# Kernel optimization log

Measured on AMD Instinct MI355X. Metric: run time of the kernel, lower is better.

## Reference

```python
import jax, jax.numpy as jnp
import numpy as np

N_NODES = 100000
N_EDGES = 3200000
IN_DIM, HID_DIM, OUT_DIM = 384, 128, 5


def gcn_conv(x, src, dst, W, b, num_nodes):
    # PyG GCNConv: add self-loops, symmetric normalization, linear, aggregate, bias
    h = x @ W  # [N, out]
    ones = jnp.ones(src.shape[0], dtype=h.dtype)
    deg = jax.ops.segment_sum(ones, dst, num_segments=num_nodes)  # includes self-loops
    dinv = jnp.where(deg > 0, jax.lax.rsqrt(deg), 0.0)
    norm = dinv[src] * dinv[dst]  # [E+N]
    msg = h[src] * norm[:, None]
    out = jax.ops.segment_sum(msg, dst, num_segments=num_nodes)
    return out + b


def setup_inputs() -> dict:
    key = jax.random.key(0)
    ks = jax.random.split(key, 8)
    x = jax.random.normal(ks[0], (N_NODES, IN_DIM), dtype=jnp.float32)
    edge_index = jax.random.randint(ks[1], (2, N_EDGES), 0, N_NODES, dtype=jnp.int64)
    # Glorot-ish init for GCN linear weights
    def glorot(k, fi, fo):
        s = jnp.sqrt(6.0 / (fi + fo))
        return jax.random.uniform(k, (fi, fo), jnp.float32, -s, s)
    W1 = glorot(ks[2], IN_DIM, HID_DIM)
    b1 = jnp.zeros((HID_DIM,), jnp.float32)
    W2 = glorot(ks[3], HID_DIM, HID_DIM)
    b2 = jnp.zeros((HID_DIM,), jnp.float32)
    W3 = glorot(ks[4], HID_DIM, OUT_DIM)
    b3 = jnp.zeros((OUT_DIM,), jnp.float32)
    return {"x": x, "edge_index": edge_index, "W1": W1, "b1": b1,
            "W2": W2, "b2": b2, "W3": W3, "b3": b3}


def reference(x, edge_index, W1, b1, W2, b2, W3, b3):
    num_nodes = x.shape[0]
    loops = jnp.arange(num_nodes, dtype=edge_index.dtype)
    src = jnp.concatenate([edge_index[0], loops])
    dst = jnp.concatenate([edge_index[1], loops])
    # layer 1: GCNConv + ReLU (dropout is identity at inference)
    h = jax.nn.relu(gcn_conv(x, src, dst, W1, b1, num_nodes))
    # layer 2
    h = jax.nn.relu(gcn_conv(h, src, dst, W2, b2, num_nodes))
    # final layer: logits, no activation
    return gcn_conv(h, src, dst, W3, b3, num_nodes)
```

## Files before the change

kernel.cpp:

```cpp
#include <hip/hip_runtime.h>

#define NN 100000
#define NE 3200000
#define SCAN_CHUNK 1024

#define BSH 8
#define BKT_NODES 256
#define NBKT ((NN + BKT_NODES - 1) / BKT_NODES)
#define BIN_BLOCKS 256
#define EPB ((NE + BIN_BLOCKS - 1) / BIN_BLOCKS)
#define GH (NBKT * BIN_BLOCKS)

typedef unsigned int uint;
typedef unsigned short ushort;
typedef __attribute__((ext_vector_type(8))) short short8;
typedef __attribute__((ext_vector_type(4))) float f32x4;

__device__ inline ushort bf16rne(float x) {
    uint u = __float_as_uint(x);
    u += 0x7FFFu + ((u >> 16) & 1u);
    return (ushort)(u >> 16);
}
__device__ inline void split2(float x, ushort& h, ushort& l) {
    h = bf16rne(x);
    float hf = __uint_as_float((uint)h << 16);
    l = bf16rne(x - hf);
}
__device__ inline uint bf16pair(float a, float b) {
    uint ua = __float_as_uint(a);
    uint ub = __float_as_uint(b);
    ua += 0x7FFFu + ((ua >> 16) & 1u);
    ub += 0x7FFFu + ((ub >> 16) & 1u);
    return (ua >> 16) | (ub & 0xFFFF0000u);
}
__device__ inline float bflo(uint u) { return __uint_as_float(u << 16); }
__device__ inline float bfhi(uint u) { return __uint_as_float(u & 0xFFFF0000u); }

__global__ __launch_bounds__(256) void hist_bkt(const int* __restrict__ dst,
                                                int* __restrict__ ghist) {
    __shared__ int h[NBKT];
    int t = threadIdx.x;
    for (int i = t; i < NBKT; i += 256) h[i] = 0;
    __syncthreads();
    int beg = blockIdx.x * EPB;
    int end = beg + EPB; if (end > NE) end = NE;
    for (int e = beg + t; e < end; e += 256)
        atomicAdd(&h[dst[e] >> BSH], 1);
    __syncthreads();
    for (int i = t; i < NBKT; i += 256)
        ghist[i * BIN_BLOCKS + blockIdx.x] = h[i];
}

__global__ __launch_bounds__(256) void scan_p1(const int* __restrict__ cnt,
                                               int* __restrict__ bsum, int N) {
    int t = threadIdx.x;
    int base = blockIdx.x * SCAN_CHUNK + t * 4;
    int s = 0;
#pragma unroll
    for (int q = 0; q < 4; q++) {
        int i = base + q;
        if (i < N) s += cnt[i];
    }
    __shared__ int red[4];
#pragma unroll
    for (int off = 32; off; off >>= 1) s += __shfl_down(s, off, 64);
    if ((t & 63) == 0) red[t >> 6] = s;
    __syncthreads();
    if (t == 0) bsum[blockIdx.x] = red[0] + red[1] + red[2] + red[3];
}

__global__ void scan_p2(int* __restrict__ bsum, int nb) {
    __shared__ int s[128];
    int t = threadIdx.x;
    int v = (t < nb) ? bsum[t] : 0;
    s[t] = v;
    __syncthreads();
    for (int off = 1; off < 128; off <<= 1) {
        int x = s[t];
        int add = (t >= off) ? s[t - off] : 0;
        __syncthreads();
        s[t] = x + add;
        __syncthreads();
    }
    if (t < nb) bsum[t] = s[t] - v;
}

__global__ __launch_bounds__(256) void scan_p3_plain(int* __restrict__ data,
                                                     const int* __restrict__ bsum, int N) {
    __shared__ int ts[256];
    int t = threadIdx.x;
    int base = blockIdx.x * SCAN_CHUNK + t * 4;
    int c[4];
    int s = 0;
#pragma unroll
    for (int q = 0; q < 4; q++) {
        int i = base + q;
        c[q] = (i < N) ? data[i] : 0;
        s += c[q];
    }
    ts[t] = s;
    __syncthreads();
    for (int off = 1; off < 256; off <<= 1) {
        int x = ts[t];
        int add = (t >= off) ? ts[t - off] : 0;
        __syncthreads();
        ts[t] = x + add;
        __syncthreads();
    }
    int run = bsum[blockIdx.x] + ts[t] - s;
#pragma unroll
    for (int q = 0; q < 4; q++) {
        int i = base + q;
        if (i < N) { data[i] = run; run += c[q]; }
    }
}

__global__ __launch_bounds__(256) void scan_p3_deg(const int* __restrict__ cnt,
                                                   const int* __restrict__ bsum,
                                                   int* __restrict__ rowptr,
                                                   float* __restrict__ dinv, int N) {
    __shared__ int ts[256];
    int t = threadIdx.x;
    int base = blockIdx.x * SCAN_CHUNK + t * 4;
    int c[4];
    int s = 0;
#pragma unroll
    for (int q = 0; q < 4; q++) {
        int i = base + q;
        c[q] = (i < N) ? cnt[i] : 0;
        s += c[q];
    }
    ts[t] = s;
    __syncthreads();
    for (int off = 1; off < 256; off <<= 1) {
        int x = ts[t];
        int add = (t >= off) ? ts[t - off] : 0;
        __syncthreads();
        ts[t] = x + add;
        __syncthreads();
    }
    int run = bsum[blockIdx.x] + ts[t] - s;
#pragma unroll
    for (int q = 0; q < 4; q++) {
        int i = base + q;
        if (i < N) {
            rowptr[i] = run;
            dinv[i] = 1.0f / sqrtf((float)(c[q] + 1));
            run += c[q];
        }
    }
    if (base < N && N <= base + 4) rowptr[N] = run;
}

__global__ __launch_bounds__(256) void bin_edges(const int* __restrict__ src,
                                                 const int* __restrict__ dst,
                                                 const int* __restrict__ ghist,
                                                 uint* __restrict__ binned) {
    __shared__ int cur[NBKT];
    int t = threadIdx.x;
    for (int i = t; i < NBKT; i += 256) cur[i] = ghist[i * BIN_BLOCKS + blockIdx.x];
    __syncthreads();
    int beg = blockIdx.x * EPB;
    int end = beg + EPB; if (end > NE) end = NE;
    for (int e = beg + t; e < end; e += 256) {
        int d = dst[e];
        int b = d >> BSH;
        int p = atomicAdd(&cur[b], 1);
        binned[p] = ((uint)src[e] << BSH) | (uint)(d & (BKT_NODES - 1));
    }
}

__global__ __launch_bounds__(256) void bucket_count(const uint* __restrict__ binned,
                                                    const int* __restrict__ ghist,
                                                    int* __restrict__ cnt) {
    __shared__ int c[BKT_NODES];
    int t = threadIdx.x;
    int bkt = blockIdx.x;
    for (int i = t; i < BKT_NODES; i += 256) c[i] = 0;
    __syncthreads();
    int beg = ghist[bkt * BIN_BLOCKS];
    int end = (bkt == NBKT - 1) ? NE : ghist[(bkt + 1) * BIN_BLOCKS];
    for (int j = beg + t; j < end; j += 256)
        atomicAdd(&c[binned[j] & (BKT_NODES - 1)], 1);
    __syncthreads();
    int base = bkt * BKT_NODES;
    int nb = NN - base; if (nb > BKT_NODES) nb = BKT_NODES;
    for (int i = t; i < nb; i += 256) cnt[base + i] = c[i];
}

__global__ __launch_bounds__(256) void csr_fill(const uint* __restrict__ binned,
                                                const int* __restrict__ ghist,
                                                const int* __restrict__ rowptr,
                                                int* __restrict__ col) {
    __shared__ int fill[BKT_NODES];
    int t = threadIdx.x;
    int bkt = blockIdx.x;
    for (int i = t; i < BKT_NODES; i += 256) fill[i] = 0;
    __syncthreads();
    int beg = ghist[bkt * BIN_BLOCKS];
    int end = (bkt == NBKT - 1) ? NE : ghist[(bkt + 1) * BIN_BLOCKS];
    int base = bkt * BKT_NODES;
    for (int j = beg + t; j < end; j += 256) {
        uint r = binned[j];
        int dl = r & (BKT_NODES - 1);
        int p = rowptr[base + dl] + atomicAdd(&fill[dl], 1);
        col[p] = (int)(r >> BSH);
    }
}

template <int K>
__global__ __launch_bounds__(256) void wsplit(const float* __restrict__ W,
                                              ushort* __restrict__ Wth,
                                              ushort* __restrict__ Wtl) {
    __shared__ float tile[32][128];
    int t = threadIdx.x;
    int kb = blockIdx.x;
    {
        int k = t >> 3, cq = t & 7;
#pragma unroll
        for (int q = 0; q < 4; q++) {
            float4 v = *(const float4*)&W[(size_t)(kb * 32 + k) * 128 + cq * 16 + q * 4];
            *(float4*)&tile[k][cq * 16 + q * 4] = v;
        }
    }
    __syncthreads();
    {
        int c = t >> 1, g = t & 1;
        ushort hs[16], ls[16];
#pragma unroll
        for (int i = 0; i < 16; i++) split2(tile[g * 16 + i][c], hs[i], ls[i]);
        uint h[8], lo[8];
#pragma unroll
        for (int i = 0; i < 8; i++) {
            h[i] = (uint)hs[2 * i] | ((uint)hs[2 * i + 1] << 16);
            lo[i] = (uint)ls[2 * i] | ((uint)ls[2 * i + 1] << 16);
        }
        size_t o = (size_t)c * K + kb * 32 + g * 16;
        *(uint4*)&Wth[o] = make_uint4(h[0], h[1], h[2], h[3]);
        *(uint4*)&Wth[o + 8] = make_uint4(h[4], h[5], h[6], h[7]);
        *(uint4*)&Wtl[o] = make_uint4(lo[0], lo[1], lo[2], lo[3]);
        *(uint4*)&Wtl[o + 8] = make_uint4(lo[4], lo[5], lo[6], lo[7]);
    }
}

template <int K>
__global__ __launch_bounds__(256) void mfma_gemm(const float* __restrict__ X,
                                                 const ushort* __restrict__ Wth,
                                                 const ushort* __restrict__ Wtl,
                                                 const float* __restrict__ dinv,
                                                 uint* __restrict__ Y, int M) {
    __shared__ char smem[24 * 1024];
    char* aHi = smem;
    char* aLo = smem + 4096;
    char* bHi = smem + 8192;
    char* bLo = smem + 16384;
    int tid = threadIdx.x;
    int w = tid >> 6, l = tid & 63;
    int rowBase = blockIdx.x * 64;

    f32x4 acc[8];
#pragma unroll
    for (int n = 0; n < 8; n++) acc[n] = (f32x4){0.f, 0.f, 0.f, 0.f};

    int sRow = tid >> 2, sKg = tid & 3;
    int gRowA = rowBase + sRow;
    int fKg = l >> 4;
    int aOff = fKg * 1024 + ((16 * w + (l & 15)) ^ fKg) * 16;

    for (int kt = 0; kt < K; kt += 32) {
        {
            float v[8];
            if (gRowA < M) {
                float4 p0 = *(const float4*)&X[(size_t)gRowA * K + kt + sKg * 8];
                float4 p1 = *(const float4*)&X[(size_t)gRowA * K + kt + sKg * 8 + 4];
                v[0] = p0.x; v[1] = p0.y; v[2] = p0.z; v[3] = p0.w;
                v[4] = p1.x; v[5] = p1.y; v[6] = p1.z; v[7] = p1.w;
            } else {
#pragma unroll
                for (int i = 0; i < 8; i++) v[i] = 0.f;
            }
            uint hh[4], hl[4];
#pragma unroll
            for (int i = 0; i < 4; i++) {
                ushort h0, l0, h1, l1;
                split2(v[2 * i], h0, l0);
                split2(v[2 * i + 1], h1, l1);
                hh[i] = (uint)h0 | ((uint)h1 << 16);
                hl[i] = (uint)l0 | ((uint)l1 << 16);
            }
            int wa = sKg * 1024 + ((sRow ^ sKg) * 16);
            *(uint4*)(aHi + wa) = make_uint4(hh[0], hh[1], hh[2], hh[3]);
            *(uint4*)(aLo + wa) = make_uint4(hl[0], hl[1], hl[2], hl[3]);
        }
#pragma unroll
        for (int i = 0; i < 2; i++) {
            int ci = tid + i * 256;
            int colb = ci >> 2, kg = ci & 3;
            uint4 vh = *(const uint4*)&Wth[(size_t)colb * K + kt + kg * 8];
            uint4 vl = *(const uint4*)&Wtl[(size_t)colb * K + kt + kg * 8];
            int wb = kg * 2048 + ((colb ^ kg) * 16);
            *(uint4*)(bHi + wb) = vh;
            *(uint4*)(bLo + wb) = vl;
        }
        __syncthreads();
        short8 ah = *(const short8*)(aHi + aOff);
        short8 al = *(const short8*)(aLo + aOff);
#pragma unroll
        for (int n = 0; n < 8; n++) {
            int bOff = fKg * 2048 + ((16 * n + (l & 15)) ^ fKg) * 16;
            short8 bh = *(const short8*)(bHi + bOff);
            short8 bl = *(const short8*)(bLo + bOff);
            acc[n] = __builtin_amdgcn_mfma_f32_16x16x32_bf16(ah, bh, acc[n], 0, 0, 0);
            acc[n] = __builtin_amdgcn_mfma_f32_16x16x32_bf16(ah, bl, acc[n], 0, 0, 0);
            acc[n] = __builtin_amdgcn_mfma_f32_16x16x32_bf16(al, bh, acc[n], 0, 0, 0);
        }
        __syncthreads();
    }
    float dscale[4];
#pragma unroll
    for (int r = 0; r < 4; r++) {
        int row = rowBase + 16 * w + (l >> 4) * 4 + r;
        dscale[r] = (row < M) ? dinv[row] : 0.f;
    }
#pragma unroll
    for (int n = 0; n < 8; n++) {
#pragma unroll
        for (int r = 0; r < 4; r++) {
            float val = acc[n][r] * dscale[r];
            float p = __shfl_xor(val, 1, 64);
            int row = rowBase + 16 * w + (l >> 4) * 4 + r;
            if (!(l & 1) && row < M)
                Y[(size_t)row * 64 + 8 * n + ((l & 15) >> 1)] = bf16pair(val, p);
        }
    }
}

__global__ void gemm_n5(const float* __restrict__ X, const float* __restrict__ W,
                        float* __restrict__ Y, int M) {
    int idx = blockIdx.x * 256 + threadIdx.x;
    int row = idx / 5, c = idx % 5;
    if (row >= M) return;
    float acc = 0.f;
#pragma unroll 8
    for (int k = 0; k < 128; k++) acc += X[row * 128 + k] * W[k * 5 + c];
    Y[row * 5 + c] = acc;
}

__global__ void pack5(const float* __restrict__ Y, const float* __restrict__ dinv,
                      uint4* __restrict__ hc, int N) {
    int node = blockIdx.x * 256 + threadIdx.x;
    if (node >= N) return;
    float di = dinv[node];
    float v0 = Y[node * 5 + 0] * di;
    float v1 = Y[node * 5 + 1] * di;
    float v2 = Y[node * 5 + 2] * di;
    float v3 = Y[node * 5 + 3] * di;
    float v4 = Y[node * 5 + 4] * di;
    hc[node] = make_uint4(bf16pair(v0, v1), bf16pair(v2, v3), bf16pair(v4, 0.f), 0u);
}

#define ACC8(v)                         \
    a0 += bflo(v.x); a1 += bfhi(v.x);   \
    a2 += bflo(v.y); a3 += bfhi(v.y);   \
    a4 += bflo(v.z); a5 += bfhi(v.z);   \
    a6 += bflo(v.w); a7 += bfhi(v.w);

__global__ __launch_bounds__(256) void agg128_v3(const uint4* __restrict__ hb4,
                                                 const int* __restrict__ rowptr,
                                                 const int* __restrict__ col,
                                                 const float* __restrict__ dinv,
                                                 const float* __restrict__ bias,
                                                 float* __restrict__ out, int N, int do_relu) {
    int wave = threadIdx.x >> 6;
    int lane = threadIdx.x & 63;
    int node = blockIdx.x * 4 + wave;
    if (node >= N) return;
    int g = lane >> 4;
    int q = lane & 15;
    int beg = rowptr[node], end = rowptr[node + 1];
    float a0 = 0.f, a1 = 0.f, a2 = 0.f, a3 = 0.f, a4 = 0.f, a5 = 0.f, a6 = 0.f, a7 = 0.f;

    int j = beg;
    for (; j + 16 <= end; j += 16) {
        int s0 = col[j + g];
        int s1 = col[j + 4 + g];
        int s2 = col[j + 8 + g];
        int s3 = col[j + 12 + g];
        uint4 v0 = hb4[(size_t)s0 * 16 + q];
        uint4 v1 = hb4[(size_t)s1 * 16 + q];
        uint4 v2 = hb4[(size_t)s2 * 16 + q];
        uint4 v3 = hb4[(size_t)s3 * 16 + q];
        ACC8(v0); ACC8(v1); ACC8(v2); ACC8(v3);
    }
    if (j + 8 <= end) {
        int s0 = col[j + g];
        int s1 = col[j + 4 + g];
        uint4 v0 = hb4[(size_t)s0 * 16 + q];
        uint4 v1 = hb4[(size_t)s1 * 16 + q];
        ACC8(v0); ACC8(v1);
        j += 8;
    }
    if (j < end) {
        int jj0 = j + g, jj1 = j + 4 + g;
        bool p0 = jj0 < end, p1 = jj1 < end;
        int s0 = p0 ? col[jj0] : node;
        int s1 = p1 ? col[jj1] : node;
        uint4 v0 = hb4[(size_t)s0 * 16 + q];
        uint4 v1 = hb4[(size_t)s1 * 16 + q];
        if (!p0) v0 = make_uint4(0u, 0u, 0u, 0u);
        if (!p1) v1 = make_uint4(0u, 0u, 0u, 0u);
        ACC8(v0); ACC8(v1);
    }
#pragma unroll
    for (int off = 16; off <= 32; off <<= 1) {
        a0 += __shfl_xor(a0, off, 64);
        a1 += __shfl_xor(a1, off, 64);
        a2 += __shfl_xor(a2, off, 64);
        a3 += __shfl_xor(a3, off, 64);
        a4 += __shfl_xor(a4, off, 64);
        a5 += __shfl_xor(a5, off, 64);
        a6 += __shfl_xor(a6, off, 64);
        a7 += __shfl_xor(a7, off, 64);
    }
    if (g == 0) {
        uint4 vs = hb4[(size_t)node * 16 + q];
        ACC8(vs);
        float di = dinv[node];
        const float4* bias4 = (const float4*)bias;
        float4 bb0 = bias4[q * 2], bb1 = bias4[q * 2 + 1];
        float o0 = a0 * di + bb0.x, o1 = a1 * di + bb0.y;
        float o2 = a2 * di + bb0.z, o3 = a3 * di + bb0.w;
        float o4 = a4 * di + bb1.x, o5 = a5 * di + bb1.y;
        float o6 = a6 * di + bb1.z, o7 = a7 * di + bb1.w;
        if (do_relu) {
            o0 = fmaxf(o0, 0.f); o1 = fmaxf(o1, 0.f);
            o2 = fmaxf(o2, 0.f); o3 = fmaxf(o3, 0.f);
            o4 = fmaxf(o4, 0.f); o5 = fmaxf(o5, 0.f);
            o6 = fmaxf(o6, 0.f); o7 = fmaxf(o7, 0.f);
        }
        float4* out4 = (float4*)out;
        out4[(size_t)node * 32 + q * 2] = make_float4(o0, o1, o2, o3);
        out4[(size_t)node * 32 + q * 2 + 1] = make_float4(o4, o5, o6, o7);
    }
}

__global__ void agg5_v2(const uint4* __restrict__ hc, const int* __restrict__ rowptr,
                        const int* __restrict__ col, const float* __restrict__ dinv,
                        const float* __restrict__ b3, float* __restrict__ out, int N) {
    int node = blockIdx.x * 256 + threadIdx.x;
    if (node >= N) return;
    float a0 = 0.f, a1 = 0.f, a2 = 0.f, a3 = 0.f, a4 = 0.f;
    int beg = rowptr[node], end = rowptr[node + 1];
#pragma unroll 2
    for (int j = beg; j < end; ++j) {
        uint4 v = hc[col[j]];
        a0 += bflo(v.x); a1 += bfhi(v.x);
        a2 += bflo(v.y); a3 += bfhi(v.y);
        a4 += bflo(v.z);
    }
    uint4 vs = hc[node];
    a0 += bflo(vs.x); a1 += bfhi(vs.x);
    a2 += bflo(vs.y); a3 += bfhi(vs.y);
    a4 += bflo(vs.z);
    float di = dinv[node];
    out[node * 5 + 0] = a0 * di + b3[0];
    out[node * 5 + 1] = a1 * di + b3[1];
    out[node * 5 + 2] = a2 * di + b3[2];
    out[node * 5 + 3] = a3 * di + b3[3];
    out[node * 5 + 4] = a4 * di + b3[4];
}

static inline size_t align512(size_t x) { return (x + 511) & ~(size_t)511; }

extern "C" void kernel_launch(void* const* d_in, const int* in_sizes, int n_in,
                              void* d_out, int out_size, void* d_ws, size_t ws_size,
                              hipStream_t stream) {
    const float* x  = (const float*)d_in[0];
    const int* ei   = (const int*)d_in[1];
    const float* W1 = (const float*)d_in[2];
    const float* b1 = (const float*)d_in[3];
    const float* W2 = (const float*)d_in[4];
    const float* b2 = (const float*)d_in[5];
    const float* W3 = (const float*)d_in[6];
    const float* b3 = (const float*)d_in[7];
    const int* src = ei;
    const int* dst = ei + NE;

    char* ws = (char*)d_ws;
    size_t off = 0;
    int* cnt = (int*)(ws + off);        off += align512((size_t)NN * 4);
    int* rowptr = (int*)(ws + off);     off += align512((size_t)(NN + 1) * 4);
    float* dinv = (float*)(ws + off);   off += align512((size_t)NN * 4);
    int* bsum = (int*)(ws + off);       off += align512((size_t)128 * 4);
    int* ghist = (int*)(ws + off);      off += align512((size_t)GH * 4);
    ushort* wt1h = (ushort*)(ws + off); off += align512((size_t)128 * 384 * 2);
    ushort* wt1l = (ushort*)(ws + off); off += align512((size_t)128 * 384 * 2);
    ushort* wt2h = (ushort*)(ws + off); off += align512((size_t)128 * 128 * 2);
    ushort* wt2l = (ushort*)(ws + off); off += align512((size_t)128 * 128 * 2);
    int* col = (int*)(ws + off);        off += align512((size_t)NE * 4);
    uint* hb = (uint*)(ws + off);       off += align512((size_t)NN * 64 * 4);
    float* bufF = (float*)(ws + off);   off += align512((size_t)NN * 128 * 4);
    float* bufC = (float*)(ws + off);   off += align512((size_t)NN * 5 * 4);
    uint4* hc = (uint4*)(ws + off);     off += align512((size_t)NN * 16);
    uint* binned = (uint*)bufF;
    (void)ws_size;

    wsplit<384><<<12, 256, 0, stream>>>(W1, wt1h, wt1l);
    wsplit<128><<<4, 256, 0, stream>>>(W2, wt2h, wt2l);

    hist_bkt<<<BIN_BLOCKS, 256, 0, stream>>>(dst, ghist);
    {
        int nb = (GH + SCAN_CHUNK - 1) / SCAN_CHUNK;
        scan_p1<<<nb, 256, 0, stream>>>(ghist, bsum, GH);
        scan_p2<<<1, 128, 0, stream>>>(bsum, nb);
        scan_p3_plain<<<nb, 256, 0, stream>>>(ghist, bsum, GH);
    }
    bin_edges<<<BIN_BLOCKS, 256, 0, stream>>>(src, dst, ghist, binned);
    bucket_count<<<NBKT, 256, 0, stream>>>(binned, ghist, cnt);
    {
        int nb = (NN + SCAN_CHUNK - 1) / SCAN_CHUNK;
        scan_p1<<<nb, 256, 0, stream>>>(cnt, bsum, NN);
        scan_p2<<<1, 128, 0, stream>>>(bsum, nb);
        scan_p3_deg<<<nb, 256, 0, stream>>>(cnt, bsum, rowptr, dinv, NN);
    }
    csr_fill<<<NBKT, 256, 0, stream>>>(binned, ghist, rowptr, col);

    int gemm_blocks = (NN + 63) / 64;
    mfma_gemm<384><<<gemm_blocks, 256, 0, stream>>>(x, wt1h, wt1l, dinv, hb, NN);
    agg128_v3<<<(NN + 3) / 4, 256, 0, stream>>>((const uint4*)hb, rowptr, col, dinv, b1, bufF, NN, 1);
    mfma_gemm<128><<<gemm_blocks, 256, 0, stream>>>(bufF, wt2h, wt2l, dinv, hb, NN);
    agg128_v3<<<(NN + 3) / 4, 256, 0, stream>>>((const uint4*)hb, rowptr, col, dinv, b2, bufF, NN, 1);
    gemm_n5<<<((NN * 5) + 255) / 256, 256, 0, stream>>>(bufF, W3, bufC, NN);
    pack5<<<(NN + 255) / 256, 256, 0, stream>>>(bufC, dinv, hc, NN);
    agg5_v2<<<(NN + 255) / 256, 256, 0, stream>>>(hc, rowptr, col, dinv, b3, (float*)d_out, NN);
}
```

Measured before the change: 492.3 us.

## Enlarge GEMM row tile, prefetch A into registers, load B via global_load_lds

The split-bf16 MFMA GEMM now processes 128 rows per block, so each wave computes two 16-row fragments and every B fragment read from LDS is reused twice. The next A k-slice is prefetched into registers while MFMAs run. B tiles are copied straight from global memory into LDS with global_load_lds instead of passing through registers. The XOR swizzle is dropped in favour of an unswizzled layout, which may add LDS bank conflicts, and the larger LDS footprint and accumulator count could lower occupancy.

Measured after the change: 495.9 us. No clear change (+0.7%).

```diff
diff --git a/kernel.cpp b/kernel.cpp
--- a/kernel.cpp
+++ b/kernel.cpp
@@ -15,6 +15,12 @@
 typedef unsigned short ushort;
 typedef __attribute__((ext_vector_type(8))) short short8;
 typedef __attribute__((ext_vector_type(4))) float f32x4;
+
+__device__ inline void gload16(const void* g, void* l) {
+    __builtin_amdgcn_global_load_lds(
+        (const __attribute__((address_space(1))) void*)g,
+        (__attribute__((address_space(3))) void*)l, 16, 0, 0);
+}
 
 __device__ inline ushort bf16rne(float x) {
     uint u = __float_as_uint(x);
@@ -249,88 +255,111 @@
                                                  const ushort* __restrict__ Wtl,
                                                  const float* __restrict__ dinv,
                                                  uint* __restrict__ Y, int M) {
-    __shared__ char smem[24 * 1024];
+    __shared__ char smem[32 * 1024];
     char* aHi = smem;
-    char* aLo = smem + 4096;
-    char* bHi = smem + 8192;
-    char* bLo = smem + 16384;
+    char* aLo = smem + 8192;
+    char* bHi = smem + 16384;
+    char* bLo = smem + 24576;
     int tid = threadIdx.x;
     int w = tid >> 6, l = tid & 63;
-    int rowBase = blockIdx.x * 64;
-
-    f32x4 acc[8];
-#pragma unroll
-    for (int n = 0; n < 8; n++) acc[n] = (f32x4){0.f, 0.f, 0.f, 0.f};
-
-    int sRow = tid >> 2, sKg = tid & 3;
-    int gRowA = rowBase + sRow;
-    int fKg = l >> 4;
-    int aOff = fKg * 1024 + ((16 * w + (l & 15)) ^ fKg) * 16;
+    int rowBase = blockIdx.x * 128;
+
+    f32x4 acc[2][8];
+#pragma unroll
+    for (int mf = 0; mf < 2; mf++)
+#pragma unroll
+        for (int n = 0; n < 8; n++) acc[mf][n] = (f32x4){0.f, 0.f, 0.f, 0.f};
+
+    int sRow = tid >> 1, sKp = tid & 1;
+    int gRow = rowBase + sRow;
+    bool rowOK = gRow < M;
+    size_t aBase = (size_t)(rowOK ? gRow : 0) * K + sKp * 16;
+
+    float4 a0, a1, a2, a3;
+    a0 = a1 = a2 = a3 = make_float4(0.f, 0.f, 0.f, 0.f);
+    if (rowOK) {
+        a0 = *(const float4*)&X[aBase];
+        a1 = *(const float4*)&X[aBase + 4];
+        a2 = *(const float4*)&X[aBase + 8];
+        a3 = *(const float4*)&X[aBase + 12];
+    }
+
+    int fc = l & 15, fkg = l >> 4;
 
     for (int kt = 0; kt < K; kt += 32) {
+#pragma unroll
+        for (int i = 0; i < 2; i++) {
+            int cb = (i * 4 + w) * 64;
+            int c = cb + l;
+            int colb = c >> 2, kg = c & 3;
+            size_t go = (size_t)colb * K + kt + kg * 8;
+            gload16(&Wth[go], bHi + cb * 16);
+            gload16(&Wtl[go], bLo + cb * 16);
+        }
         {
-            float v[8];
-            if (gRowA < M) {
-                float4 p0 = *(const float4*)&X[(size_t)gRowA * K + kt + sKg * 8];
-                float4 p1 = *(const float4*)&X[(size_t)gRowA * K + kt + sKg * 8 + 4];
-                v[0] = p0.x; v[1] = p0.y; v[2] = p0.z; v[3] = p0.w;
-                v[4] = p1.x; v[5] = p1.y; v[6] = p1.z; v[7] = p1.w;
-            } else {
-#pragma unroll
-                for (int i = 0; i < 8; i++) v[i] = 0.f;
-            }
-            uint hh[4], hl[4];
-#pragma unroll
-            for (int i = 0; i < 4; i++) {
+            float v[16] = {a0.x, a0.y, a0.z, a0.w, a1.x, a1.y, a1.z, a1.w,
+                           a2.x, a2.y, a2.z, a2.w, a3.x, a3.y, a3.z, a3.w};
+            uint hh[8], hl[8];
+#pragma unroll
+            for (int i = 0; i < 8; i++) {
                 ushort h0, l0, h1, l1;
                 split2(v[2 * i], h0, l0);
                 split2(v[2 * i + 1], h1, l1);
                 hh[i] = (uint)h0 | ((uint)h1 << 16);
                 hl[i] = (uint)l0 | ((uint)l1 << 16);
             }
-            int wa = sKg * 1024 + ((sRow ^ sKg) * 16);
+            int wa = (sRow * 4 + sKp * 2) * 16;
             *(uint4*)(aHi + wa) = make_uint4(hh[0], hh[1], hh[2], hh[3]);
+            *(uint4*)(aHi + wa + 16) = make_uint4(hh[4], hh[5], hh[6], hh[7]);
             *(uint4*)(aLo + wa) = make_uint4(hl[0], hl[1], hl[2], hl[3]);
-        }
-#pragma unroll
-        for (int i = 0; i < 2; i++) {
-            int ci = tid + i * 256;
-            int colb = ci >> 2, kg = ci & 3;
-            uint4 vh = *(const uint4*)&Wth[(size_t)colb * K + kt + kg * 8];
-            uint4 vl = *(const uint4*)&Wtl[(size_t)colb * K + kt + kg * 8];
-            int wb = kg * 2048 + ((colb ^ kg) * 16);
-            *(uint4*)(bHi + wb) = vh;
-            *(uint4*)(bLo + wb) = vl;
-        }
-        __syncthreads();
-        short8 ah = *(const short8*)(aHi + aOff);
-        short8 al = *(const short8*)(aLo + aOff);
+            *(uint4*)(aLo + wa + 16) = make_uint4(hl[4], hl[5], hl[6], hl[7]);
+        }
+        __syncthreads();
+
+        if (kt + 32 < K && rowOK) {
+            size_t nb = aBase + kt + 32;
+            a0 = *(const float4*)&X[nb];
+            a1 = *(const float4*)&X[nb + 4];
+            a2 = *(const float4*)&X[nb + 8];
+            a3 = *(const float4*)&X[nb + 12];
+        }
+
+#pragma unroll
+        for (int mf = 0; mf < 2; mf++) {
+            int aoff = (((2 * w + mf) * 16 + fc) * 4 + fkg) * 16;
+            short8 ah = *(const short8*)(aHi + aoff);
+            short8 al = *(const short8*)(aLo + aoff);
+#pragma unroll
+            for (int n = 0; n < 8; n++) {
+                int boff = ((16 * n + fc) * 4 + fkg) * 16;
+                short8 bh = *(const short8*)(bHi + boff);
+                short8 bl = *(const short8*)(bLo + boff);
+                acc[mf][n] = __builtin_amdgcn_mfma_f32_16x16x32_bf16(ah, bh, acc[mf][n], 0, 0, 0);
+                acc[mf][n] = __builtin_amdgcn_mfma_f32_16x16x32_bf16(ah, bl, acc[mf][n], 0, 0, 0);
+                acc[mf][n] = __builtin_amdgcn_mfma_f32_16x16x32_bf16(al, bh, acc[mf][n], 0, 0, 0);
+            }
+        }
+        __syncthreads();
+    }
+
+#pragma unroll
+    for (int mf = 0; mf < 2; mf++) {
+        float dscale[4];
+#pragma unroll
+        for (int r = 0; r < 4; r++) {
+            int row = rowBase + (2 * w + mf) * 16 + fkg * 4 + r;
+            dscale[r] = (row < M) ? dinv[row] : 0.f;
+        }
 #pragma unroll
         for (int n = 0; n < 8; n++) {
-            int bOff = fKg * 2048 + ((16 * n + (l & 15)) ^ fKg) * 16;
-            short8 bh = *(const short8*)(bHi + bOff);
-            short8 bl = *(const short8*)(bLo + bOff);
-            acc[n] = __builtin_amdgcn_mfma_f32_16x16x32_bf16(ah, bh, acc[n], 0, 0, 0);
-            acc[n] = __builtin_amdgcn_mfma_f32_16x16x32_bf16(ah, bl, acc[n], 0, 0, 0);
-            acc[n] = __builtin_amdgcn_mfma_f32_16x16x32_bf16(al, bh, acc[n], 0, 0, 0);
-        }
-        __syncthreads();
-    }
-    float dscale[4];
-#pragma unroll
-    for (int r = 0; r < 4; r++) {
-        int row = rowBase + 16 * w + (l >> 4) * 4 + r;
-        dscale[r] = (row < M) ? dinv[row] : 0.f;
-    }
-#pragma unroll
-    for (int n = 0; n < 8; n++) {
-#pragma unroll
-        for (int r = 0; r < 4; r++) {
-            float val = acc[n][r] * dscale[r];
-            float p = __shfl_xor(val, 1, 64);
-            int row = rowBase + 16 * w + (l >> 4) * 4 + r;
-            if (!(l & 1) && row < M)
-                Y[(size_t)row * 64 + 8 * n + ((l & 15) >> 1)] = bf16pair(val, p);
+#pragma unroll
+            for (int r = 0; r < 4; r++) {
+                float val = acc[mf][n][r] * dscale[r];
+                float p = __shfl_xor(val, 1, 64);
+                int row = rowBase + (2 * w + mf) * 16 + fkg * 4 + r;
+                if (!(l & 1) && row < M)
+                    Y[(size_t)row * 64 + 8 * n + (fc >> 1)] = bf16pair(val, p);
+            }
         }
     }
 }
@@ -525,7 +554,7 @@
     }
     csr_fill<<<NBKT, 256, 0, stream>>>(binned, ghist, rowptr, col);
 
-    int gemm_blocks = (NN + 63) / 64;
+    int gemm_blocks = (NN + 127) / 128;
     mfma_gemm<384><<<gemm_blocks, 256, 0, stream>>>(x, wt1h, wt1l, dinv, hb, NN);
     agg128_v3<<<(NN + 3) / 4, 256, 0, stream>>>((const uint4*)hb, rowptr, col, dinv, b1, bufF, NN, 1);
     mfma_gemm<128><<<gemm_blocks, 256, 0, stream>>>(bufF, wt2h, wt2l, dinv, hb, NN);
```
